# Optimization experiments

Measured on AMD Instinct MI355X. Metric: run time of the kernel, lower is better.

Reference implementation:

```python
import jax, jax.numpy as jnp
import numpy as np

B, T, K = 256, 512, 128

def setup_inputs() -> dict:
    key = jax.random.key(0)
    k1, k2, k3, k4, k5 = jax.random.split(key, 5)
    emissions = jax.random.normal(k1, (B, T, K), dtype=jnp.float32)
    tags = jax.random.randint(k2, (B, T), 0, K)
    mask = jnp.ones((B, T), dtype=bool)
    # xavier_uniform_ for trans: limit = sqrt(6/(fan_in+fan_out))
    limit = float(np.sqrt(6.0 / (K + K)))
    trans = jax.random.uniform(k3, (K, K), minval=-limit, maxval=limit, dtype=jnp.float32)
    start = 0.1 * jax.random.normal(k4, (K,), dtype=jnp.float32)
    end = 0.1 * jax.random.normal(k5, (K,), dtype=jnp.float32)
    return {"emissions": emissions, "trans": trans, "start": start, "end": end,
            "tags": tags, "mask": mask}

def reference(emissions, trans, start, end, tags, mask):
    # --- log partition (forward algorithm) via lax.scan over time ---
    em_t = jnp.moveaxis(emissions, 1, 0)  # [T,B,K]
    mk_t = jnp.moveaxis(mask, 1, 0)       # [T,B]
    alpha0 = start + em_t[0]              # [B,K]

    def step(alpha, xs):
        em, mk = xs                                      # em:[B,K], mk:[B]
        scores = alpha[:, :, None] + trans[None] + em[:, None, :]  # [B,K,K]
        alpha_next = jax.nn.logsumexp(scores, axis=1)    # [B,K]
        alpha = jnp.where(mk[:, None], alpha_next, alpha)
        return alpha, None

    alpha, _ = jax.lax.scan(step, alpha0, (em_t[1:], mk_t[1:]))
    logZ = jax.nn.logsumexp(alpha + end, axis=1)  # [B]

    # --- gold path score, fully vectorized ---
    emit = jnp.take_along_axis(emissions, tags[..., None], axis=2)[..., 0]  # [B,T]
    trans_sc = trans[tags[:, :-1], tags[:, 1:]]                             # [B,T-1]
    step_sc = (emit[:, 1:] + trans_sc) * mask[:, 1:]                        # masked steps
    score = start[tags[:, 0]] + emit[:, 0] + jnp.sum(step_sc, axis=1)
    last_idx = jnp.sum(mask, axis=1).astype(jnp.int32) - 1
    last_tags = jnp.take_along_axis(tags, last_idx[:, None], axis=1)[:, 0]
    score = score + end[last_tags]

    return jnp.mean(logZ - score)
```

## Files before the change

### kernel.cpp

```cpp
#include <hip/hip_runtime.h>

#define B_ 256
#define T_ 512
#define K_ 128

typedef _Float16 half2_t __attribute__((ext_vector_type(2)));
typedef unsigned uvec16 __attribute__((ext_vector_type(16)));

__device__ inline float fast_exp2(float x) {
#if __has_builtin(__builtin_amdgcn_exp2f)
    return __builtin_amdgcn_exp2f(x);
#else
    return exp2f(x);
#endif
}
__device__ inline float fast_log2(float x) {
#if __has_builtin(__builtin_amdgcn_logf)
    return __builtin_amdgcn_logf(x);
#else
    return log2f(x);
#endif
}
__device__ inline float dot2(half2_t a, half2_t b, float c) {
#if __has_builtin(__builtin_amdgcn_fdot2)
    return __builtin_amdgcn_fdot2(a, b, c, false);
#else
    return fmaf((float)a.x, (float)b.x, fmaf((float)a.y, (float)b.y, c));
#endif
}
__device__ inline unsigned pack2(float x, float y) {
#if __has_builtin(__builtin_amdgcn_cvt_pkrtz)
    auto h = __builtin_amdgcn_cvt_pkrtz(x, y);
    return __builtin_bit_cast(unsigned, h);
#else
    half2_t h; h.x = (_Float16)x; h.y = (_Float16)y;
    return __builtin_bit_cast(unsigned, h);
#endif
}
__device__ inline half2_t as_h2(unsigned u) {
    return __builtin_bit_cast(half2_t, u);
}

#define WS_TT   0
#define WS_FV   (K_ * K_)
#define WS_BV   (WS_FV + B_ * 64)
#define WS_M2F  (WS_BV + B_ * 64)
#define WS_M2B  (WS_M2F + B_)
#define WS_SC   (WS_M2B + B_)

__global__ void crf_transpose_kernel(const float* __restrict__ trans,
                                     float* __restrict__ transT)
{
    int idx = blockIdx.x * 256 + threadIdx.x;
    int r = idx >> 7, c = idx & (K_ - 1);
    transT[c * K_ + r] = trans[r * K_ + c];
}


__global__ __launch_bounds__(256, 1)
void crf_half_kernel(const float* __restrict__ emissions,
                     const float* __restrict__ trans,
                     const float* __restrict__ start,
                     const float* __restrict__ endv,
                     const int* __restrict__ tags,
                     unsigned* __restrict__ ws_u32)
{
    const int bid  = blockIdx.x;
    const bool fwd = bid < B_;
    const int b    = fwd ? bid : bid - B_;
    const int tid  = threadIdx.x;
    const int wave = tid >> 6;
    const int lane = tid & 63;
    const int q    = lane >> 4;
    const int cp   = (lane & 15) + (wave << 4);
    const int j0   = cp << 1;
    const int j1   = j0 + 1;
    const int i0   = q << 5;

    __shared__ __align__(16) _Float16 aebuf[2][K_];
    __shared__ __align__(16) _Float16 emlds[256][K_];
    __shared__ float wred[4];

    const float* transT = (const float*)(ws_u32 + WS_TT);
    unsigned*    fv     = ws_u32 + WS_FV;
    unsigned*    bv     = ws_u32 + WS_BV;
    float*       m2f    = (float*)(ws_u32 + WS_M2F);
    float*       m2b    = (float*)(ws_u32 + WS_M2B);
    float*       scp    = (float*)(ws_u32 + WS_SC);

    const float* eb = emissions + (size_t)b * T_ * K_;
    const int*   tg = tags + b * T_;

    const float L  = 1.44269504f;
    const float C2 = 7.7f;

    const float* M = fwd ? trans : transT;
    const int NIT  = fwd ? (T_ / 2 - 1) : (T_ / 2);

    {
        const int rbase = fwd ? 0 : 256;
        const float4* ef4 = reinterpret_cast<const float4*>(eb + (size_t)rbase * K_);
        #pragma unroll
        for (int it = 0; it < 32; it += 16) {
            float4 tmp[16];
            #pragma unroll
            for (int u = 0; u < 16; ++u)
                tmp[u] = ef4[(it + u) * 256 + tid];
            #pragma unroll
            for (int u = 0; u < 16; ++u) {
                int f = (it + u) * 256 + tid;
                int r = f >> 5, m = f & 31;
                uint2 w;
                w.x = pack2(tmp[u].x, tmp[u].y);
                w.y = pack2(tmp[u].z, tmp[u].w);
                *reinterpret_cast<uint2*>(&emlds[r][4 * m]) = w;
            }
        }
    }

    uvec16 e0, e1;
    #pragma unroll
    for (int r = 0; r < 4; ++r) {
        #pragma unroll
        for (int c = 0; c < 4; ++c) {
            int ii = i0 + 8 * r + 2 * c;
            e0[4*r+c] = pack2(fast_exp2(M[ii * K_ + j0] * L),
                              fast_exp2(M[(ii + 1) * K_ + j0] * L));
            e1[4*r+c] = pack2(fast_exp2(M[ii * K_ + j1] * L),
                              fast_exp2(M[(ii + 1) * K_ + j1] * L));
        }
    }

    __syncthreads();

    float2 sv = fwd ? *reinterpret_cast<const float2*>(&start[j0])
                    : *reinterpret_cast<const float2*>(&endv[j0]);
    half2_t ei = as_h2(*reinterpret_cast<const unsigned*>(&emlds[fwd ? 0 : 255][j0]));
    float z0 = (sv.x + (float)ei.x) * L;
    float z1 = (sv.y + (float)ei.y) * L;
    float m0 = fmaxf(z0, z1);
    #pragma unroll
    for (int d = 1; d < 64; d <<= 1) m0 = fmaxf(m0, __shfl_xor(m0, d));
    if (lane == 0) wred[wave] = m0;
    __syncthreads();
    float M2 = fmaxf(fmaxf(wred[0], wred[1]), fmaxf(wred[2], wred[3]));
    float aen0 = fast_exp2(z0 - M2);
    float aen1 = fast_exp2(z1 - M2);
    if (q == 0)
        *reinterpret_cast<unsigned*>(&aebuf[0][j0]) = pack2(aen0, aen1);
    __syncthreads();

    const int em_base = fwd ? 0 : (T_ / 2 - 1);
    const int em_sign = fwd ? 1 : -1;

    for (int n = 1; n <= NIT; ++n) {
        const _Float16* aerow = aebuf[(n - 1) & 1];
        const uint4* aeq = reinterpret_cast<const uint4*>(aerow + i0);
        uint2 pr = *reinterpret_cast<const uint2*>(aerow);

        const int emrow = em_base + em_sign * n;
        float em0v = 0.f, em1v = 0.f;
        if (emrow >= 0) {
            half2_t eh = as_h2(*reinterpret_cast<const unsigned*>(&emlds[emrow][j0]));
            em0v = (float)eh.x; em1v = (float)eh.y;
        }

        float a00 = 0.f, a01 = 0.f, a10 = 0.f, a11 = 0.f;
        #pragma unroll
        for (int r = 0; r < 4; ++r) {
            uint4 v = aeq[r];
            int p = r * 4;
            a00 = dot2(as_h2(v.x), as_h2(e0[p + 0]), a00);
            a01 = dot2(as_h2(v.y), as_h2(e0[p + 1]), a01);
            a00 = dot2(as_h2(v.z), as_h2(e0[p + 2]), a00);
            a01 = dot2(as_h2(v.w), as_h2(e0[p + 3]), a01);
            a10 = dot2(as_h2(v.x), as_h2(e1[p + 0]), a10);
            a11 = dot2(as_h2(v.y), as_h2(e1[p + 1]), a11);
            a10 = dot2(as_h2(v.z), as_h2(e1[p + 2]), a10);
            a11 = dot2(as_h2(v.w), as_h2(e1[p + 3]), a11);
        }

        half2_t q0 = as_h2(pr.x), q1 = as_h2(pr.y);
        float pm = fmaxf(fmaxf((float)q0.x, (float)q0.y),
                         fmaxf((float)q1.x, (float)q1.y));
        pm = fmaxf(pm, 6.1e-5f);
        float corr = fast_log2(pm);
        float F0 = fast_exp2(fmaf(em0v, L, -C2 - corr));
        float F1 = fast_exp2(fmaf(em1v, L, -C2 - corr));

        float s0 = a00 + a01;
        float s1 = a10 + a11;
        s0 += __shfl_xor(s0, 16); s1 += __shfl_xor(s1, 16);
        s0 += __shfl_xor(s0, 32); s1 += __shfl_xor(s1, 32);

        aen0 = s0 * F0;
        aen1 = s1 * F1;
        M2 += C2 + corr;

        if (q == 0)
            *reinterpret_cast<unsigned*>(&aebuf[n & 1][j0]) = pack2(aen0, aen1);
        __syncthreads();
    }

    if (q == 0)
        (fwd ? fv : bv)[b * 64 + cp] = pack2(aen0, aen1);
    if (tid == 0)
        (fwd ? m2f : m2b)[b] = M2;

    if (fwd) {
        float sc = 0.0f;
        for (int k = tid; k < T_; k += 256) {
            int cur = tg[k];
            sc += eb[(size_t)k * K_ + cur];
            if (k > 0) sc += trans[tg[k - 1] * K_ + cur];
        }
        #pragma unroll
        for (int d = 1; d < 64; d <<= 1) sc += __shfl_xor(sc, d);
        __syncthreads();
        if (lane == 0) wred[wave] = sc;
        __syncthreads();
        if (tid == 0)
            scp[b] = wred[0] + wred[1] + wred[2] + wred[3]
                   + start[tg[0]] + endv[tg[T_ - 1]];
    }
}

__global__ void crf_join_kernel(const unsigned* __restrict__ ws_u32,
                                float* __restrict__ out)
{
    const unsigned* fv  = ws_u32 + WS_FV;
    const unsigned* bv  = ws_u32 + WS_BV;
    const float*    m2f = (const float*)(ws_u32 + WS_M2F);
    const float*    m2b = (const float*)(ws_u32 + WS_M2B);
    const float*    scp = (const float*)(ws_u32 + WS_SC);

    const float LN2 = 0.69314718f;
    int b = threadIdx.x;

    float acc = 0.0f;
    #pragma unroll
    for (int k = 0; k < 64; ++k)
        acc = dot2(as_h2(fv[b * 64 + k]), as_h2(bv[b * 64 + k]), acc);

    float logZ = (m2f[b] + m2b[b] + fast_log2(acc)) * LN2;
    float v = logZ - scp[b];

    #pragma unroll
    for (int d = 1; d < 64; d <<= 1) v += __shfl_xor(v, d);
    __shared__ float w[4];
    if ((threadIdx.x & 63) == 0) w[threadIdx.x >> 6] = v;
    __syncthreads();
    if (threadIdx.x == 0)
        out[0] = (w[0] + w[1] + w[2] + w[3]) * (1.0f / 256.0f);
}

extern "C" void kernel_launch(void* const* d_in, const int* in_sizes, int n_in,
                              void* d_out, int out_size, void* d_ws, size_t ws_size,
                              hipStream_t stream)
{
    const float* emissions = (const float*)d_in[0];
    const float* trans     = (const float*)d_in[1];
    const float* start     = (const float*)d_in[2];
    const float* endv      = (const float*)d_in[3];
    const int*   tags      = (const int*)d_in[4];

    unsigned* ws = (unsigned*)d_ws;

    crf_transpose_kernel<<<K_ * K_ / 256, 256, 0, stream>>>(trans, (float*)(ws + WS_TT));
    crf_half_kernel<<<2 * B_, 256, 0, stream>>>(emissions, trans, start, endv, tags, ws);
    crf_join_kernel<<<1, 256, 0, stream>>>(ws, (float*)d_out);
}
```

Before: 126.2 us.

## Use MFMA for the forward/backward recurrence, pairing two sequences per block

```diff
diff --git a/kernel.cpp b/kernel.cpp
--- a/kernel.cpp
+++ b/kernel.cpp
@@ -3,9 +3,11 @@
 #define B_ 256
 #define T_ 512
 #define K_ 128
-
+#define HALF_T 256
+
+typedef _Float16 half8 __attribute__((ext_vector_type(8)));
 typedef _Float16 half2_t __attribute__((ext_vector_type(2)));
-typedef unsigned uvec16 __attribute__((ext_vector_type(16)));
+typedef float f32x4 __attribute__((ext_vector_type(4)));
 
 __device__ inline float fast_exp2(float x) {
 #if __has_builtin(__builtin_amdgcn_exp2f)
@@ -66,19 +68,18 @@
                      unsigned* __restrict__ ws_u32)
 {
     const int bid  = blockIdx.x;
-    const bool fwd = bid < B_;
-    const int b    = fwd ? bid : bid - B_;
+    const bool fwd = bid < (B_ / 2);
+    const int bp   = fwd ? bid : bid - (B_ / 2);
+    const int b0g  = bp * 2;
     const int tid  = threadIdx.x;
     const int wave = tid >> 6;
     const int lane = tid & 63;
-    const int q    = lane >> 4;
-    const int cp   = (lane & 15) + (wave << 4);
-    const int j0   = cp << 1;
-    const int j1   = j0 + 1;
-    const int i0   = q << 5;
-
-    __shared__ __align__(16) _Float16 aebuf[2][K_];
-    __shared__ __align__(16) _Float16 emlds[256][K_];
+    const int l15  = lane & 15;
+    const int g4   = lane >> 4;
+    const int colbase = (wave << 5) + l15;
+
+    __shared__ __align__(16) _Float16 emlds[2][HALF_T][K_];
+    __shared__ __align__(16) _Float16 aebuf[2][2][160];
     __shared__ float wred[4];
 
     const float* transT = (const float*)(ws_u32 + WS_TT);
@@ -88,140 +89,161 @@
     float*       m2b    = (float*)(ws_u32 + WS_M2B);
     float*       scp    = (float*)(ws_u32 + WS_SC);
 
-    const float* eb = emissions + (size_t)b * T_ * K_;
-    const int*   tg = tags + b * T_;
-
     const float L  = 1.44269504f;
     const float C2 = 7.7f;
-
-    const float* M = fwd ? trans : transT;
-    const int NIT  = fwd ? (T_ / 2 - 1) : (T_ / 2);
+    const float LN2 = 0.69314718f;
+
+    const float* M   = fwd ? trans : transT;
+    const float* sv_ = fwd ? start : endv;
+    const int rbase  = fwd ? 0 : HALF_T;
+    const int r0     = fwd ? 0 : (HALF_T - 1);
+    const int NIT    = fwd ? (HALF_T - 1) : HALF_T;
+    const int em_base = fwd ? 0 : (HALF_T - 1);
+    const int em_sign = fwd ? 1 : -1;
+
+    for (int b = 0; b < 2; ++b) {
+        const float4* ef4 = reinterpret_cast<const float4*>(
+            emissions + ((size_t)(b0g + b) * T_ + rbase) * K_);
+        for (int it = 0; it < 32; ++it) {
+            int f = it * 256 + tid;
+            float4 v = ef4[f];
+            int r = f >> 5, m = f & 31;
+            uint2 w;
+            w.x = pack2(v.x, v.y);
+            w.y = pack2(v.z, v.w);
+            *reinterpret_cast<uint2*>(&emlds[b][r][4 * m]) = w;
+        }
+    }
+
+#define EFRAG(kc, nc, dst)                                                  \
+    {                                                                       \
+        half8 t;                                                            \
+        _Pragma("unroll")                                                   \
+        for (int i = 0; i < 8; ++i) {                                       \
+            int k = (kc) * 32 + g4 * 8 + i;                                 \
+            t[i] = (_Float16)fast_exp2(M[k * K_ + colbase + 16 * (nc)] * L);\
+        }                                                                   \
+        dst = t;                                                            \
+    }
+    half8 e00, e01, e10, e11, e20, e21, e30, e31;
+    EFRAG(0, 0, e00) EFRAG(0, 1, e01)
+    EFRAG(1, 0, e10) EFRAG(1, 1, e11)
+    EFRAG(2, 0, e20) EFRAG(2, 1, e21)
+    EFRAG(3, 0, e30) EFRAG(3, 1, e31)
+#undef EFRAG
+
+    __syncthreads();
 
     {
-        const int rbase = fwd ? 0 : 256;
-        const float4* ef4 = reinterpret_cast<const float4*>(eb + (size_t)rbase * K_);
+        int ib = tid >> 7, ij = tid & 127;
+        float z = (sv_[ij] + (float)emlds[ib][r0][ij]) * L;
+        float mx = z;
         #pragma unroll
-        for (int it = 0; it < 32; it += 16) {
-            float4 tmp[16];
+        for (int d = 1; d < 64; d <<= 1) mx = fmaxf(mx, __shfl_xor(mx, d));
+        if (lane == 0) wred[wave] = mx;
+    }
+    __syncthreads();
+    float M2_0 = fmaxf(wred[0], wred[1]);
+    float M2_1 = fmaxf(wred[2], wred[3]);
+    {
+        int ib = tid >> 7, ij = tid & 127;
+        float Mz = ib == 0 ? M2_0 : M2_1;
+        float z = (sv_[ij] + (float)emlds[ib][r0][ij]) * L;
+        aebuf[0][ib][ij] = (_Float16)fast_exp2(z - Mz);
+    }
+    __syncthreads();
+
+    const int bsel = lane & 1;
+    for (int n = 1; n <= NIT; ++n) {
+        const _Float16* aerow = &aebuf[(n - 1) & 1][0][0];
+
+        const char* abase = (const char*)aerow + bsel * 320 + (g4 << 4);
+        half8 a0 = *reinterpret_cast<const half8*>(abase);
+        half8 a1 = *reinterpret_cast<const half8*>(abase + 64);
+        half8 a2 = *reinterpret_cast<const half8*>(abase + 128);
+        half8 a3 = *reinterpret_cast<const half8*>(abase + 192);
+
+        uint2 p0 = *reinterpret_cast<const uint2*>(aerow);
+        uint2 p1 = *reinterpret_cast<const uint2*>(aerow + 160);
+
+        const int emrow = em_base + em_sign * n;
+        float em00 = 0.f, em01 = 0.f, em10 = 0.f, em11 = 0.f;
+        if (emrow >= 0) {
+            em00 = (float)emlds[0][emrow][colbase];
+            em01 = (float)emlds[0][emrow][colbase + 16];
+            em10 = (float)emlds[1][emrow][colbase];
+            em11 = (float)emlds[1][emrow][colbase + 16];
+        }
+
+        f32x4 acc0 = {0.f, 0.f, 0.f, 0.f};
+        f32x4 acc1 = {0.f, 0.f, 0.f, 0.f};
+        acc0 = __builtin_amdgcn_mfma_f32_16x16x32_f16(a0, e00, acc0, 0, 0, 0);
+        acc1 = __builtin_amdgcn_mfma_f32_16x16x32_f16(a0, e01, acc1, 0, 0, 0);
+        acc0 = __builtin_amdgcn_mfma_f32_16x16x32_f16(a1, e10, acc0, 0, 0, 0);
+        acc1 = __builtin_amdgcn_mfma_f32_16x16x32_f16(a1, e11, acc1, 0, 0, 0);
+        acc0 = __builtin_amdgcn_mfma_f32_16x16x32_f16(a2, e20, acc0, 0, 0, 0);
+        acc1 = __builtin_amdgcn_mfma_f32_16x16x32_f16(a2, e21, acc1, 0, 0, 0);
+        acc0 = __builtin_amdgcn_mfma_f32_16x16x32_f16(a3, e30, acc0, 0, 0, 0);
+        acc1 = __builtin_amdgcn_mfma_f32_16x16x32_f16(a3, e31, acc1, 0, 0, 0);
+
+        half2_t q0 = as_h2(p0.x), q1 = as_h2(p0.y);
+        float pm0 = fmaxf(fmaxf((float)q0.x, (float)q0.y),
+                          fmaxf((float)q1.x, (float)q1.y));
+        half2_t r0h = as_h2(p1.x), r1h = as_h2(p1.y);
+        float pm1 = fmaxf(fmaxf((float)r0h.x, (float)r0h.y),
+                          fmaxf((float)r1h.x, (float)r1h.y));
+        pm0 = fmaxf(pm0, 6.1e-5f);
+        pm1 = fmaxf(pm1, 6.1e-5f);
+        float corr0 = fast_log2(pm0);
+        float corr1 = fast_log2(pm1);
+
+        float F00 = fast_exp2(fmaf(em00, L, -C2 - corr0));
+        float F01 = fast_exp2(fmaf(em01, L, -C2 - corr0));
+        float F10 = fast_exp2(fmaf(em10, L, -C2 - corr1));
+        float F11 = fast_exp2(fmaf(em11, L, -C2 - corr1));
+
+        if (g4 == 0) {
+            _Float16* nb = &aebuf[n & 1][0][0];
+            nb[colbase]            = (_Float16)(acc0[0] * F00);
+            nb[colbase + 16]       = (_Float16)(acc1[0] * F01);
+            nb[160 + colbase]      = (_Float16)(acc0[1] * F10);
+            nb[160 + colbase + 16] = (_Float16)(acc1[1] * F11);
+        }
+        M2_0 += C2 + corr0;
+        M2_1 += C2 + corr1;
+        __syncthreads();
+    }
+
+    {
+        int ib = tid >> 7, ij = tid & 127;
+        _Float16 v = aebuf[NIT & 1][ib][ij];
+        unsigned short* dst = (unsigned short*)(fwd ? fv : bv);
+        dst[(size_t)(b0g + ib) * 128 + ij] = __builtin_bit_cast(unsigned short, v);
+    }
+    if (tid == 0) {
+        (fwd ? m2f : m2b)[b0g]     = M2_0;
+        (fwd ? m2f : m2b)[b0g + 1] = M2_1;
+    }
+
+    if (fwd) {
+        for (int bi = 0; bi < 2; ++bi) {
+            const int*   tg = tags + (size_t)(b0g + bi) * T_;
+            const float* eb = emissions + (size_t)(b0g + bi) * T_ * K_;
+            float sc = 0.0f;
+            for (int k = tid; k < T_; k += 256) {
+                int cur = tg[k];
+                sc += eb[(size_t)k * K_ + cur];
+                if (k > 0) sc += trans[tg[k - 1] * K_ + cur];
+            }
             #pragma unroll
-            for (int u = 0; u < 16; ++u)
-                tmp[u] = ef4[(it + u) * 256 + tid];
-            #pragma unroll
-            for (int u = 0; u < 16; ++u) {
-                int f = (it + u) * 256 + tid;
-                int r = f >> 5, m = f & 31;
-                uint2 w;
-                w.x = pack2(tmp[u].x, tmp[u].y);
-                w.y = pack2(tmp[u].z, tmp[u].w);
-                *reinterpret_cast<uint2*>(&emlds[r][4 * m]) = w;
-            }
-        }
-    }
-
-    uvec16 e0, e1;
-    #pragma unroll
-    for (int r = 0; r < 4; ++r) {
-        #pragma unroll
-        for (int c = 0; c < 4; ++c) {
-            int ii = i0 + 8 * r + 2 * c;
-            e0[4*r+c] = pack2(fast_exp2(M[ii * K_ + j0] * L),
-                              fast_exp2(M[(ii + 1) * K_ + j0] * L));
-            e1[4*r+c] = pack2(fast_exp2(M[ii * K_ + j1] * L),
-                              fast_exp2(M[(ii + 1) * K_ + j1] * L));
-        }
-    }
-
-    __syncthreads();
-
-    float2 sv = fwd ? *reinterpret_cast<const float2*>(&start[j0])
-                    : *reinterpret_cast<const float2*>(&endv[j0]);
-    half2_t ei = as_h2(*reinterpret_cast<const unsigned*>(&emlds[fwd ? 0 : 255][j0]));
-    float z0 = (sv.x + (float)ei.x) * L;
-    float z1 = (sv.y + (float)ei.y) * L;
-    float m0 = fmaxf(z0, z1);
-    #pragma unroll
-    for (int d = 1; d < 64; d <<= 1) m0 = fmaxf(m0, __shfl_xor(m0, d));
-    if (lane == 0) wred[wave] = m0;
-    __syncthreads();
-    float M2 = fmaxf(fmaxf(wred[0], wred[1]), fmaxf(wred[2], wred[3]));
-    float aen0 = fast_exp2(z0 - M2);
-    float aen1 = fast_exp2(z1 - M2);
-    if (q == 0)
-        *reinterpret_cast<unsigned*>(&aebuf[0][j0]) = pack2(aen0, aen1);
-    __syncthreads();
-
-    const int em_base = fwd ? 0 : (T_ / 2 - 1);
-    const int em_sign = fwd ? 1 : -1;
-
-    for (int n = 1; n <= NIT; ++n) {
-        const _Float16* aerow = aebuf[(n - 1) & 1];
-        const uint4* aeq = reinterpret_cast<const uint4*>(aerow + i0);
-        uint2 pr = *reinterpret_cast<const uint2*>(aerow);
-
-        const int emrow = em_base + em_sign * n;
-        float em0v = 0.f, em1v = 0.f;
-        if (emrow >= 0) {
-            half2_t eh = as_h2(*reinterpret_cast<const unsigned*>(&emlds[emrow][j0]));
-            em0v = (float)eh.x; em1v = (float)eh.y;
-        }
-
-        float a00 = 0.f, a01 = 0.f, a10 = 0.f, a11 = 0.f;
-        #pragma unroll
-        for (int r = 0; r < 4; ++r) {
-            uint4 v = aeq[r];
-            int p = r * 4;
-            a00 = dot2(as_h2(v.x), as_h2(e0[p + 0]), a00);
-            a01 = dot2(as_h2(v.y), as_h2(e0[p + 1]), a01);
-            a00 = dot2(as_h2(v.z), as_h2(e0[p + 2]), a00);
-            a01 = dot2(as_h2(v.w), as_h2(e0[p + 3]), a01);
-            a10 = dot2(as_h2(v.x), as_h2(e1[p + 0]), a10);
-            a11 = dot2(as_h2(v.y), as_h2(e1[p + 1]), a11);
-            a10 = dot2(as_h2(v.z), as_h2(e1[p + 2]), a10);
-            a11 = dot2(as_h2(v.w), as_h2(e1[p + 3]), a11);
-        }
-
-        half2_t q0 = as_h2(pr.x), q1 = as_h2(pr.y);
-        float pm = fmaxf(fmaxf((float)q0.x, (float)q0.y),
-                         fmaxf((float)q1.x, (float)q1.y));
-        pm = fmaxf(pm, 6.1e-5f);
-        float corr = fast_log2(pm);
-        float F0 = fast_exp2(fmaf(em0v, L, -C2 - corr));
-        float F1 = fast_exp2(fmaf(em1v, L, -C2 - corr));
-
-        float s0 = a00 + a01;
-        float s1 = a10 + a11;
-        s0 += __shfl_xor(s0, 16); s1 += __shfl_xor(s1, 16);
-        s0 += __shfl_xor(s0, 32); s1 += __shfl_xor(s1, 32);
-
-        aen0 = s0 * F0;
-        aen1 = s1 * F1;
-        M2 += C2 + corr;
-
-        if (q == 0)
-            *reinterpret_cast<unsigned*>(&aebuf[n & 1][j0]) = pack2(aen0, aen1);
-        __syncthreads();
-    }
-
-    if (q == 0)
-        (fwd ? fv : bv)[b * 64 + cp] = pack2(aen0, aen1);
-    if (tid == 0)
-        (fwd ? m2f : m2b)[b] = M2;
-
-    if (fwd) {
-        float sc = 0.0f;
-        for (int k = tid; k < T_; k += 256) {
-            int cur = tg[k];
-            sc += eb[(size_t)k * K_ + cur];
-            if (k > 0) sc += trans[tg[k - 1] * K_ + cur];
-        }
-        #pragma unroll
-        for (int d = 1; d < 64; d <<= 1) sc += __shfl_xor(sc, d);
-        __syncthreads();
-        if (lane == 0) wred[wave] = sc;
-        __syncthreads();
-        if (tid == 0)
-            scp[b] = wred[0] + wred[1] + wred[2] + wred[3]
-                   + start[tg[0]] + endv[tg[T_ - 1]];
+            for (int d = 1; d < 64; d <<= 1) sc += __shfl_xor(sc, d);
+            __syncthreads();
+            if (lane == 0) wred[wave] = sc;
+            __syncthreads();
+            if (tid == 0)
+                scp[b0g + bi] = wred[0] + wred[1] + wred[2] + wred[3]
+                              + start[tg[0]] + endv[tg[T_ - 1]];
+        }
     }
 }
 
@@ -267,6 +289,6 @@
     unsigned* ws = (unsigned*)d_ws;
 
     crf_transpose_kernel<<<K_ * K_ / 256, 256, 0, stream>>>(trans, (float*)(ws + WS_TT));
-    crf_half_kernel<<<2 * B_, 256, 0, stream>>>(emissions, trans, start, endv, tags, ws);
+    crf_half_kernel<<<B_, 256, 0, stream>>>(emissions, trans, start, endv, tags, ws);
     crf_join_kernel<<<1, 256, 0, stream>>>(ws, (float*)d_out);
 }
```

Result: faster. 114.1 us (-9.6%).
